# Kernel tuning notes

Measured on AMD Instinct MI355X. Metric: run time of the kernel, lower is better.

## Reference

```python
import jax, jax.numpy as jnp
import numpy as np

B, N, H, D2 = 2, 2048, 16, 64


def setup_inputs() -> dict:
    key = jax.random.key(0)
    k1, k2, k3 = jax.random.split(key, 3)
    keys = jax.random.normal(k1, (B, N, H, D2), dtype=jnp.float32)
    queries = jax.random.normal(k2, (B, N, H, D2), dtype=jnp.float32)
    values = jax.random.normal(k3, (B, N, H, D2), dtype=jnp.float32)
    return {"keys": keys, "queries": queries, "values": values}


def reference(keys, queries, values):
    b, n, h, d2 = keys.shape
    # Faithful to the original: torch uses .reshape (NOT transpose) to go
    # (b, n, h, d2) -> (b, h, n, d2), a pure memory reinterpretation.
    q = queries.reshape(b, h, n, d2)
    k = keys.reshape(b, h, n, d2)
    v = values.reshape(b, h, n, d2)
    scale = 1.0 / (d2 ** 0.5)
    # [b, h, n, n] attention scores
    scores = jnp.einsum('bhqd,bhkd->bhqk', q, k) * scale
    # causal mask: upper triangle (diagonal=1) set to -inf
    causal = jnp.triu(jnp.ones((n, n), dtype=bool), k=1)
    scores = jnp.where(causal, -jnp.inf, scores)
    attn = jax.nn.softmax(scores, axis=-1)
    out = jnp.einsum('bhqk,bhkd->bhqd', attn, v)
    return out.reshape(b, n, h, d2)
```

## Files before the change

### kernel.cpp

```cpp
#include <hip/hip_runtime.h>


typedef short  short4v __attribute__((ext_vector_type(4)));
typedef short  short8v __attribute__((ext_vector_type(8)));
typedef float  float4v __attribute__((ext_vector_type(4)));
typedef float  float8v __attribute__((ext_vector_type(8)));

#define NQ 2048
#define DD 64
#define QT 64
#define KT 64
#define KP 72
#define VP 72
#define NPAIR 16

union U2 { unsigned int u[2]; short4v s; };
union U4 { unsigned int u[4]; short8v s; };

static __device__ __forceinline__ unsigned int pktr(float lo, float hi) {
    return __builtin_amdgcn_perm(__builtin_bit_cast(unsigned int, hi),
                                 __builtin_bit_cast(unsigned int, lo),
                                 0x07060302);
}
static __device__ __forceinline__ unsigned int pkrn(float lo, float hi) {
    unsigned int a = __builtin_bit_cast(unsigned int, hi) + 0x8000u;
    unsigned int b = __builtin_bit_cast(unsigned int, lo) + 0x8000u;
    return __builtin_amdgcn_perm(a, b, 0x07060302);
}

static __device__ __forceinline__ short8v pk8t(float8v f) {
    U4 w;
#pragma unroll
    for (int i = 0; i < 4; ++i) w.u[i] = pktr(f[2 * i], f[2 * i + 1]);
    return w.s;
}

__global__ __launch_bounds__(256, 2) void mha_fwd_kernel(
    const float* __restrict__ Kg,
    const float* __restrict__ Qg,
    const float* __restrict__ Vg,
    float* __restrict__ Og)
{
    __shared__ __align__(16) unsigned short Klds[KT * KP];
    __shared__ __align__(16) unsigned short Vt[DD * VP];

    const int t    = threadIdx.x;
    const int lane = t & 63;
    const int wave = t >> 6;
    const int col  = lane & 15;
    const int quad = lane >> 4;

    const int b    = blockIdx.x;
    const int bh   = (b & 7) * 4 + ((b >> 3) & 3);
    const int pair = b >> 5;

    const size_t base = (size_t)bh * NQ * DD;
    const float* Qp = Qg + base;
    const float* Kp = Kg + base;
    const float* Vp = Vg + base;
    float*       Op = Og + base;

    const float sscale = 0.125f * 1.4426950408889634f;

    const int kr = t >> 2, kc = (t & 3) * 16;
    const int vd = t & 63, vg = (t >> 6) * 16;

    const int tiles[2] = {31 - pair, pair};

    for (int ph = 0; ph < 2; ++ph) {
        const int T    = tiles[ph];
        const int q0   = T * QT + wave * 16;
        const int qg   = q0 + col;
        const int kmax = T * QT;

        short8v qf0, qf1;
        {
            float8v a = *(const float8v*)(Qp + (size_t)(q0 + col) * DD + quad * 8);
            float8v c = *(const float8v*)(Qp + (size_t)(q0 + col) * DD + 32 + quad * 8);
            U4 w0, w1;
#pragma unroll
            for (int i = 0; i < 4; ++i) {
                w0.u[i] = pkrn(a[2 * i] * sscale, a[2 * i + 1] * sscale);
                w1.u[i] = pkrn(c[2 * i] * sscale, c[2 * i + 1] * sscale);
            }
            qf0 = w0.s;
            qf1 = w1.s;
        }

        float l_i = 0.0f;
        float4v o[4];
#pragma unroll
        for (int d = 0; d < 4; ++d) o[d] = (float4v){0.f, 0.f, 0.f, 0.f};

        float8v ka  = *(const float8v*)(Kp + (size_t)kr * DD + kc);
        float8v kb8 = *(const float8v*)(Kp + (size_t)kr * DD + kc + 8);
        float vr[16];
#pragma unroll
        for (int i = 0; i < 16; ++i) vr[i] = Vp[(size_t)(vg + i) * DD + vd];

        for (int kb = 0; kb <= kmax; kb += KT) {
            __syncthreads();

            *(short8v*)&Klds[kr * KP + kc]     = pk8t(ka);
            *(short8v*)&Klds[kr * KP + kc + 8] = pk8t(kb8);
            {
                U4 w0, w1;
#pragma unroll
                for (int i = 0; i < 4; ++i) {
                    w0.u[i] = pktr(vr[2 * i], vr[2 * i + 1]);
                    w1.u[i] = pktr(vr[8 + 2 * i], vr[9 + 2 * i]);
                }
                *(short8v*)&Vt[vd * VP + vg]     = w0.s;
                *(short8v*)&Vt[vd * VP + vg + 8] = w1.s;
            }

            __syncthreads();

            const int nkb = kb + KT;
            if (nkb <= kmax) {
                ka  = *(const float8v*)(Kp + (size_t)(nkb + kr) * DD + kc);
                kb8 = *(const float8v*)(Kp + (size_t)(nkb + kr) * DD + kc + 8);
#pragma unroll
                for (int i = 0; i < 16; ++i)
                    vr[i] = Vp[(size_t)(nkb + vg + i) * DD + vd];
            }

            float4v sT[4];
#pragma unroll
            for (int u = 0; u < 4; ++u) {
                short8v kf0 = *(const short8v*)&Klds[(u * 16 + col) * KP + quad * 8];
                short8v kf1 = *(const short8v*)&Klds[(u * 16 + col) * KP + 32 + quad * 8];
                sT[u] = (float4v){0.f, 0.f, 0.f, 0.f};
                sT[u] = __builtin_amdgcn_mfma_f32_16x16x32_bf16(kf0, qf0, sT[u], 0, 0, 0);
                sT[u] = __builtin_amdgcn_mfma_f32_16x16x32_bf16(kf1, qf1, sT[u], 0, 0, 0);
            }

            if (kb == kmax) {
#pragma unroll
                for (int u = 0; u < 4; ++u)
#pragma unroll
                    for (int r = 0; r < 4; ++r) {
                        const int key = kb + u * 16 + quad * 4 + r;
                        if (key > qg) sT[u][r] = -3.0e38f;
                    }
            }

            short4v pf[4];
#pragma unroll
            for (int u = 0; u < 4; ++u) {
#pragma unroll
                for (int r = 0; r < 4; ++r) {
                    sT[u][r] = exp2f(sT[u][r]);
                    l_i += sT[u][r];
                }
                U2 w;
                w.u[0] = pktr(sT[u][0], sT[u][1]);
                w.u[1] = pktr(sT[u][2], sT[u][3]);
                pf[u] = w.s;
            }

#pragma unroll
            for (int d = 0; d < 4; ++d) {
#pragma unroll
                for (int u = 0; u < 4; ++u) {
                    short4v vf = *(const short4v*)&Vt[(d * 16 + col) * VP + u * 16 + quad * 4];
                    o[d] = __builtin_amdgcn_mfma_f32_16x16x16bf16_1k(pf[u], vf, o[d], 0, 0, 0);
                }
            }
        }

        float rs = l_i;
        rs += __shfl_xor(rs, 16);
        rs += __shfl_xor(rs, 32);
        float lv[4];
#pragma unroll
        for (int r = 0; r < 4; ++r) lv[r] = 1.0f / __shfl(rs, quad * 4 + r, 64);
#pragma unroll
        for (int r = 0; r < 4; ++r)
#pragma unroll
            for (int d = 0; d < 4; ++d)
                Op[(size_t)(q0 + quad * 4 + r) * DD + d * 16 + col] = o[d][r] * lv[r];
    }
}

extern "C" void kernel_launch(void* const* d_in, const int* in_sizes, int n_in,
                              void* d_out, int out_size, void* d_ws, size_t ws_size,
                              hipStream_t stream) {
    const float* keys    = (const float*)d_in[0];
    const float* queries = (const float*)d_in[1];
    const float* values  = (const float*)d_in[2];
    float* out           = (float*)d_out;

    dim3 grid(2 * 16 * NPAIR);
    dim3 block(256, 1, 1);
    mha_fwd_kernel<<<grid, block, 0, stream>>>(keys, queries, values, out);
}
```

Before: 128.0 us.

## Run both causal tiles concurrently with 8 waves and double-buffered K/V LDS

The kernel no longer processes the long and short query tiles one after the other. Each block now uses 512 threads: waves 0-3 handle the long tile and waves 4-7 handle the short one, sharing a single K/V stream. K and V tiles are double-buffered in LDS and the next tile is prefetched during compute, leaving one barrier per iteration; s_setprio raises priority around the MFMA section. This removes the duplicated K/V loads and serialized phases, but the short-tile waves sit idle for most iterations, and the tighter launch bounds (512,4) may force register spills.

```diff
diff --git a/kernel.cpp b/kernel.cpp
--- a/kernel.cpp
+++ b/kernel.cpp
@@ -8,11 +8,9 @@
 
 #define NQ 2048
 #define DD 64
-#define QT 64
 #define KT 64
 #define KP 72
 #define VP 72
-#define NPAIR 16
 
 union U2 { unsigned int u[2]; short4v s; };
 union U4 { unsigned int u[4]; short8v s; };
@@ -28,21 +26,14 @@
     return __builtin_amdgcn_perm(a, b, 0x07060302);
 }
 
-static __device__ __forceinline__ short8v pk8t(float8v f) {
-    U4 w;
-#pragma unroll
-    for (int i = 0; i < 4; ++i) w.u[i] = pktr(f[2 * i], f[2 * i + 1]);
-    return w.s;
-}
-
-__global__ __launch_bounds__(256, 2) void mha_fwd_kernel(
+__global__ __launch_bounds__(512, 4) void mha_fwd_kernel(
     const float* __restrict__ Kg,
     const float* __restrict__ Qg,
     const float* __restrict__ Vg,
     float* __restrict__ Og)
 {
-    __shared__ __align__(16) unsigned short Klds[KT * KP];
-    __shared__ __align__(16) unsigned short Vt[DD * VP];
+    __shared__ __align__(16) unsigned short Klds[2][KT * KP];
+    __shared__ __align__(16) unsigned short Vt[2][DD * VP];
 
     const int t    = threadIdx.x;
     const int lane = t & 63;
@@ -50,9 +41,16 @@
     const int col  = lane & 15;
     const int quad = lane >> 4;
 
-    const int b    = blockIdx.x;
-    const int bh   = (b & 7) * 4 + ((b >> 3) & 3);
-    const int pair = b >> 5;
+    const int b  = blockIdx.x;
+    const int bh = (b & 7) * 4 + ((b >> 3) & 3);
+    const int h  = b >> 5;
+    const int p  = (h < 8) ? h : 23 - h;
+
+    const int T    = (wave < 4) ? (31 - p) : p;
+    const int q0   = T * 64 + (wave & 3) * 16;
+    const int qg   = q0 + col;
+    const int kmax = T * 64;
+    const int nt   = 32 - p;
 
     const size_t base = (size_t)bh * NQ * DD;
     const float* Qp = Qg + base;
@@ -62,74 +60,67 @@
 
     const float sscale = 0.125f * 1.4426950408889634f;
 
-    const int kr = t >> 2, kc = (t & 3) * 16;
-    const int vd = t & 63, vg = (t >> 6) * 16;
-
-    const int tiles[2] = {31 - pair, pair};
-
-    for (int ph = 0; ph < 2; ++ph) {
-        const int T    = tiles[ph];
-        const int q0   = T * QT + wave * 16;
-        const int qg   = q0 + col;
-        const int kmax = T * QT;
-
-        short8v qf0, qf1;
-        {
-            float8v a = *(const float8v*)(Qp + (size_t)(q0 + col) * DD + quad * 8);
-            float8v c = *(const float8v*)(Qp + (size_t)(q0 + col) * DD + 32 + quad * 8);
-            U4 w0, w1;
-#pragma unroll
-            for (int i = 0; i < 4; ++i) {
-                w0.u[i] = pkrn(a[2 * i] * sscale, a[2 * i + 1] * sscale);
-                w1.u[i] = pkrn(c[2 * i] * sscale, c[2 * i + 1] * sscale);
-            }
-            qf0 = w0.s;
-            qf1 = w1.s;
-        }
-
-        float l_i = 0.0f;
-        float4v o[4];
-#pragma unroll
-        for (int d = 0; d < 4; ++d) o[d] = (float4v){0.f, 0.f, 0.f, 0.f};
-
-        float8v ka  = *(const float8v*)(Kp + (size_t)kr * DD + kc);
-        float8v kb8 = *(const float8v*)(Kp + (size_t)kr * DD + kc + 8);
-        float vr[16];
-#pragma unroll
-        for (int i = 0; i < 16; ++i) vr[i] = Vp[(size_t)(vg + i) * DD + vd];
-
-        for (int kb = 0; kb <= kmax; kb += KT) {
-            __syncthreads();
-
-            *(short8v*)&Klds[kr * KP + kc]     = pk8t(ka);
-            *(short8v*)&Klds[kr * KP + kc + 8] = pk8t(kb8);
-            {
-                U4 w0, w1;
-#pragma unroll
-                for (int i = 0; i < 4; ++i) {
-                    w0.u[i] = pktr(vr[2 * i], vr[2 * i + 1]);
-                    w1.u[i] = pktr(vr[8 + 2 * i], vr[9 + 2 * i]);
-                }
-                *(short8v*)&Vt[vd * VP + vg]     = w0.s;
-                *(short8v*)&Vt[vd * VP + vg + 8] = w1.s;
-            }
-
-            __syncthreads();
-
+    const int kr = t >> 3, kc = (t & 7) * 8;
+    const int vd = t & 63, vg = (t >> 6) * 8;
+
+    short8v qf0, qf1;
+    {
+        float8v a = *(const float8v*)(Qp + (size_t)qg * DD + quad * 8);
+        float8v c = *(const float8v*)(Qp + (size_t)qg * DD + 32 + quad * 8);
+        U4 w0, w1;
+#pragma unroll
+        for (int i = 0; i < 4; ++i) {
+            w0.u[i] = pkrn(a[2 * i] * sscale, a[2 * i + 1] * sscale);
+            w1.u[i] = pkrn(c[2 * i] * sscale, c[2 * i + 1] * sscale);
+        }
+        qf0 = w0.s;
+        qf1 = w1.s;
+    }
+
+    float l_i = 0.0f;
+    float4v o[4];
+#pragma unroll
+    for (int d = 0; d < 4; ++d) o[d] = (float4v){0.f, 0.f, 0.f, 0.f};
+
+    {
+        float8v ka = *(const float8v*)(Kp + (size_t)kr * DD + kc);
+        float vr[8];
+#pragma unroll
+        for (int i = 0; i < 8; ++i) vr[i] = Vp[(size_t)(vg + i) * DD + vd];
+        U4 wk, wv;
+#pragma unroll
+        for (int i = 0; i < 4; ++i) {
+            wk.u[i] = pktr(ka[2 * i], ka[2 * i + 1]);
+            wv.u[i] = pktr(vr[2 * i], vr[2 * i + 1]);
+        }
+        *(short8v*)&Klds[0][kr * KP + kc] = wk.s;
+        *(short8v*)&Vt[0][vd * VP + vg]   = wv.s;
+    }
+    __syncthreads();
+
+    for (int it = 0; it < nt; ++it) {
+        const int cur   = it & 1;
+        const int kb    = it * KT;
+        const bool stage = (it + 1 < nt);
+
+        float8v ka;
+        float vr[8];
+        if (stage) {
             const int nkb = kb + KT;
-            if (nkb <= kmax) {
-                ka  = *(const float8v*)(Kp + (size_t)(nkb + kr) * DD + kc);
-                kb8 = *(const float8v*)(Kp + (size_t)(nkb + kr) * DD + kc + 8);
-#pragma unroll
-                for (int i = 0; i < 16; ++i)
-                    vr[i] = Vp[(size_t)(nkb + vg + i) * DD + vd];
-            }
+            ka = *(const float8v*)(Kp + (size_t)(nkb + kr) * DD + kc);
+#pragma unroll
+            for (int i = 0; i < 8; ++i)
+                vr[i] = Vp[(size_t)(nkb + vg + i) * DD + vd];
+        }
+
+        if (kb <= kmax) {
+            __builtin_amdgcn_s_setprio(1);
 
             float4v sT[4];
 #pragma unroll
             for (int u = 0; u < 4; ++u) {
-                short8v kf0 = *(const short8v*)&Klds[(u * 16 + col) * KP + quad * 8];
-                short8v kf1 = *(const short8v*)&Klds[(u * 16 + col) * KP + 32 + quad * 8];
+                short8v kf0 = *(const short8v*)&Klds[cur][(u * 16 + col) * KP + quad * 8];
+                short8v kf1 = *(const short8v*)&Klds[cur][(u * 16 + col) * KP + 32 + quad * 8];
                 sT[u] = (float4v){0.f, 0.f, 0.f, 0.f};
                 sT[u] = __builtin_amdgcn_mfma_f32_16x16x32_bf16(kf0, qf0, sT[u], 0, 0, 0);
                 sT[u] = __builtin_amdgcn_mfma_f32_16x16x32_bf16(kf1, qf1, sT[u], 0, 0, 0);
@@ -163,24 +154,39 @@
             for (int d = 0; d < 4; ++d) {
 #pragma unroll
                 for (int u = 0; u < 4; ++u) {
-                    short4v vf = *(const short4v*)&Vt[(d * 16 + col) * VP + u * 16 + quad * 4];
+                    short4v vf = *(const short4v*)&Vt[cur][(d * 16 + col) * VP + u * 16 + quad * 4];
                     o[d] = __builtin_amdgcn_mfma_f32_16x16x16bf16_1k(pf[u], vf, o[d], 0, 0, 0);
                 }
             }
-        }
-
-        float rs = l_i;
-        rs += __shfl_xor(rs, 16);
-        rs += __shfl_xor(rs, 32);
-        float lv[4];
-#pragma unroll
-        for (int r = 0; r < 4; ++r) lv[r] = 1.0f / __shfl(rs, quad * 4 + r, 64);
-#pragma unroll
-        for (int r = 0; r < 4; ++r)
-#pragma unroll
-            for (int d = 0; d < 4; ++d)
-                Op[(size_t)(q0 + quad * 4 + r) * DD + d * 16 + col] = o[d][r] * lv[r];
+
+            __builtin_amdgcn_s_setprio(0);
+        }
+
+        if (stage) {
+            U4 wk, wv;
+#pragma unroll
+            for (int i = 0; i < 4; ++i) {
+                wk.u[i] = pktr(ka[2 * i], ka[2 * i + 1]);
+                wv.u[i] = pktr(vr[2 * i], vr[2 * i + 1]);
+            }
+            *(short8v*)&Klds[cur ^ 1][kr * KP + kc] = wk.s;
+            *(short8v*)&Vt[cur ^ 1][vd * VP + vg]   = wv.s;
+        }
+
+        __syncthreads();
     }
+
+    float rs = l_i;
+    rs += __shfl_xor(rs, 16);
+    rs += __shfl_xor(rs, 32);
+    float lv[4];
+#pragma unroll
+    for (int r = 0; r < 4; ++r) lv[r] = 1.0f / __shfl(rs, quad * 4 + r, 64);
+#pragma unroll
+    for (int r = 0; r < 4; ++r)
+#pragma unroll
+        for (int d = 0; d < 4; ++d)
+            Op[(size_t)(q0 + quad * 4 + r) * DD + d * 16 + col] = o[d][r] * lv[r];
 }
 
 extern "C" void kernel_launch(void* const* d_in, const int* in_sizes, int n_in,
@@ -191,7 +197,7 @@
     const float* values  = (const float*)d_in[2];
     float* out           = (float*)d_out;
 
-    dim3 grid(2 * 16 * NPAIR);
-    dim3 block(256, 1, 1);
+    dim3 grid(2 * 16 * 16);
+    dim3 block(512, 1, 1);
     mha_fwd_kernel<<<grid, block, 0, stream>>>(keys, queries, values, out);
 }
```

After: 128.8 us. Within noise of the previous version (+0.6%).
